# Kernel optimization log

Measured on AMD Instinct MI355X. Metric: run time of the kernel, lower is better.

## Reference

```python
import jax, jax.numpy as jnp
import numpy as np

ALPHA = 2.0   # ATan surrogate alpha (spikingjelly default)
VTH = 0.5     # v_threshold
NUM_HEADS = 8

@jax.custom_vjp
def atan_spike(x):
    return (x >= 0.0).astype(x.dtype)

def _atan_fwd(x):
    return atan_spike(x), x

def _atan_bwd(x, g):
    return (g * (ALPHA / 2.0) / (1.0 + (jnp.pi / 2.0 * ALPHA * x) ** 2),)

atan_spike.defvjp(_atan_fwd, _atan_bwd)

def lif(x, w):
    # ParametricLIFNode, step_mode='m', decay_input=True, v_reset=0 (hard reset), detach_reset
    sg = jax.nn.sigmoid(w)
    def step(v, xt):
        v = v + (xt - v) * sg
        s = atan_spike(v - VTH)
        v = v * (1.0 - jax.lax.stop_gradient(s))  # hard reset to 0, detached
        return v, s
    _, spikes = jax.lax.scan(step, jnp.zeros_like(x[0]), x)
    return spikes

def bn_eT(x, gamma, beta, eps=1e-5):
    # x: [T, B, C, N]; per-(T,C) channel stats over (B, N)  == BatchNorm1d on [B, T*C, N] (train mode)
    T, B, C, N = x.shape
    mean = x.mean(axis=(1, 3), keepdims=True)
    var = jnp.mean((x - mean) ** 2, axis=(1, 3), keepdims=True)
    g = gamma.reshape(T, 1, C, 1)
    b = beta.reshape(T, 1, C, 1)
    return (x - mean) * jax.lax.rsqrt(var + eps) * g + b

def setup_inputs() -> dict:
    key = jax.random.key(0)
    ks = jax.random.split(key, 6)
    T, B, N, C = 16, 8, 196, 512
    return {
        "x": jax.random.normal(ks[0], (T, B, N, C), dtype=jnp.float32),
        "qkv_w": jax.random.normal(ks[1], (3 * C, C), dtype=jnp.float32) * 0.02,
        "qkv_b": jax.random.normal(ks[2], (3 * C,), dtype=jnp.float32) * 0.02,
        "bn1_g": jnp.ones((T * 3 * C,), dtype=jnp.float32),
        "bn1_b": jnp.zeros((T * 3 * C,), dtype=jnp.float32),
        "proj_w": jax.random.normal(ks[3], (C, C), dtype=jnp.float32) * 0.02,
        "proj_b": jax.random.normal(ks[4], (C,), dtype=jnp.float32) * 0.02,
        "bn2_g": jnp.ones((T * C,), dtype=jnp.float32),
        "bn2_b": jnp.zeros((T * C,), dtype=jnp.float32),
        "w_in": jnp.zeros((), dtype=jnp.float32),
        "w_q": jnp.zeros((), dtype=jnp.float32),
        "w_k": jnp.zeros((), dtype=jnp.float32),
        "w_v": jnp.zeros((), dtype=jnp.float32),
        "w_proj": jnp.zeros((), dtype=jnp.float32),
    }

def reference(x, qkv_w, qkv_b, bn1_g, bn1_b, proj_w, proj_b, bn2_g, bn2_b,
              w_in, w_q, w_k, w_v, w_proj):
    T, B, N, C = x.shape
    H = NUM_HEADS
    hd = C // H
    scale = hd ** -0.5

    x = lif(x, w_in)                                            # [T,B,N,C] spikes
    qkv = jnp.einsum('tbnc,oc->tbno', x, qkv_w) + qkv_b         # [T,B,N,3C]
    qkv = bn_eT(jnp.swapaxes(qkv, -2, -1), bn1_g, bn1_b)        # [T,B,3C,N]
    qkv = jnp.swapaxes(qkv, -2, -1).reshape(T, B, N, 3, H, hd)
    qkv = jnp.transpose(qkv, (3, 0, 1, 4, 2, 5))                # [3,T,B,H,N,hd]

    q_sk = lif(qkv[0], w_q)
    k_sk = lif(qkv[1], w_k)
    v_sk = lif(qkv[2], w_v)

    kv = jnp.einsum('tbhnd,tbhne->tbhde', k_sk, v_sk)           # k^T @ v : [T,B,H,hd,hd]
    out = jnp.einsum('tbhnd,tbhde->tbhne', q_sk, kv) * scale    # [T,B,H,N,hd]
    out = jnp.transpose(out, (0, 1, 3, 2, 4)).reshape(T, B, N, C)

    out = lif(out, w_proj)
    out = jnp.einsum('tbnc,oc->tbno', out, proj_w) + proj_b     # [T,B,N,C]
    out = bn_eT(jnp.swapaxes(out, -2, -1), bn2_g, bn2_b)        # [T,B,C,N]
    return jnp.swapaxes(out, -2, -1)                            # [T,B,N,C]
```

## Files before the change

### kernel.cpp

```cpp
#include <hip/hip_runtime.h>


#define TT 16
#define BB 8
#define NNQ 196
#define CC 512
#define HH 8
#define HD 64
#define O3 1536
#define BN (BB*NNQ)
#define PT (BN*CC)
#define WTOT ((O3+CC)*CC)
#define NRG 14

static constexpr float VTH = 0.5f;
typedef __attribute__((ext_vector_type(8))) short short8;
typedef __attribute__((ext_vector_type(4))) float f32x4;
typedef unsigned short u16;

__device__ __forceinline__ float sigm(float w){ return 1.f/(1.f+expf(-w)); }

__device__ __forceinline__ float lif_step(float x, float& v, float sg){
  float d  = __fsub_rn(x, v);
  float dd = __fmul_rn(d, sg);
  v = __fadd_rn(v, dd);
  float sp = (v >= VTH) ? 1.f : 0.f;
  v = __fmul_rn(v, __fsub_rn(1.f, sp));
  return sp;
}

__device__ __forceinline__ u16 bf16_rn(float x){
  unsigned u = __float_as_uint(x);
  unsigned r = u + 0x7FFF + ((u>>16)&1);
  return (u16)(r>>16);
}
__device__ __forceinline__ float bf16_to_f(u16 h){
  return __uint_as_float(((unsigned)h)<<16);
}

__device__ __forceinline__ void gld_lds16(const void* g, void* l){
  __builtin_amdgcn_global_load_lds(
    (const __attribute__((address_space(1))) unsigned int*)g,
    (__attribute__((address_space(3))) unsigned int*)l, 16, 0, 0);
}

__global__ void k_wsplit(const float* __restrict__ qkv_w, const float* __restrict__ proj_w,
                         u16* __restrict__ whi, u16* __restrict__ wmid, u16* __restrict__ wlo){
  int i = blockIdx.x*256 + threadIdx.x;
  float w = (i < O3*CC) ? qkv_w[i] : proj_w[i - O3*CC];
  u16 h = bf16_rn(w);          float r1 = w - bf16_to_f(h);
  u16 m = bf16_rn(r1);         float r2 = r1 - bf16_to_f(m);
  u16 l = bf16_rn(r2);
  whi[i]=h; wmid[i]=m; wlo[i]=l;
}

__global__ void k_lif_x(const float* __restrict__ x, const float* __restrict__ w,
                        float* __restrict__ vin, u16* __restrict__ s0, int t0, int tc){
  int g = blockIdx.x*256 + threadIdx.x;
  float sg = sigm(w[0]);
  float v = (t0==0) ? 0.f : vin[g];
  for (int tt=0; tt<tc; ++tt){
    float sp = lif_step(x[(size_t)(t0+tt)*PT + g], v, sg);
    s0[(size_t)tt*PT + g] = (sp!=0.f) ? 0x3F80 : 0;
  }
  vin[g] = v;
}

template<int ON>
__global__ __launch_bounds__(256)
void k_gemm_mfma(const u16* __restrict__ A, const u16* __restrict__ Wh,
                 const u16* __restrict__ Wm, const u16* __restrict__ Wl,
                 const float* __restrict__ bias, float* __restrict__ Cm, int M){
  __shared__ __align__(16) u16 Al[128][64];
  __shared__ __align__(16) u16 Bh[128][64];
  __shared__ __align__(16) u16 Bm[128][64];
  __shared__ __align__(16) u16 Bl[128][64];
  const int nON = ON/128;
  int nwg = gridDim.x;
  int bid = blockIdx.x;
  int q = nwg >> 3, r = nwg & 7;
  int xcd = bid & 7, idx = bid >> 3;
  int wgid = (xcd < r ? xcd*(q+1) : r*(q+1) + (xcd-r)*q) + idx;
  int mb = wgid / nON, ob = wgid - mb*nON;
  int m0 = mb*128, o0 = ob*128;

  int tid = threadIdx.x;
  int w = tid>>6, lane = tid&63;
  int wm = (w&1)*64, wn = (w>>1)*64;
  int r16 = lane&15, kg = lane>>4;
  int lrow = w*32 + (lane>>3);
  int lslot = lane&7;
  f32x4 acc[4][4] = {};
  for (int k0=0;k0<512;k0+=64){
    #pragma unroll
    for (int i=0;i<4;++i){
      int row = lrow + i*8;
      int gslot = lslot ^ (row&7);
      int gr = m0+row; if (gr>=M) gr=M-1;
      gld_lds16(&A [(size_t)gr*512       + k0 + gslot*8], &Al[w*32+i*8][0]);
      gld_lds16(&Wh[(size_t)(o0+row)*512 + k0 + gslot*8], &Bh[w*32+i*8][0]);
      gld_lds16(&Wm[(size_t)(o0+row)*512 + k0 + gslot*8], &Bm[w*32+i*8][0]);
      gld_lds16(&Wl[(size_t)(o0+row)*512 + k0 + gslot*8], &Bl[w*32+i*8][0]);
    }
    __syncthreads();
    #pragma unroll
    for (int s=0;s<2;++s){
      short8 af[4], bh[4], bm[4], bl[4];
      #pragma unroll
      for (int mt=0;mt<4;++mt){
        int rr = wm + mt*16 + r16;
        af[mt] = *(const short8*)&Al[rr][((s*4+kg)^(rr&7))*8];
      }
      #pragma unroll
      for (int nt=0;nt<4;++nt){
        int rr = wn + nt*16 + r16;
        int sl = ((s*4+kg)^(rr&7))*8;
        bh[nt] = *(const short8*)&Bh[rr][sl];
        bm[nt] = *(const short8*)&Bm[rr][sl];
        bl[nt] = *(const short8*)&Bl[rr][sl];
      }
      #pragma unroll
      for (int mt=0;mt<4;++mt)
        #pragma unroll
        for (int nt=0;nt<4;++nt){
          acc[mt][nt] = __builtin_amdgcn_mfma_f32_16x16x32_bf16(af[mt], bh[nt], acc[mt][nt],0,0,0);
          acc[mt][nt] = __builtin_amdgcn_mfma_f32_16x16x32_bf16(af[mt], bm[nt], acc[mt][nt],0,0,0);
          acc[mt][nt] = __builtin_amdgcn_mfma_f32_16x16x32_bf16(af[mt], bl[nt], acc[mt][nt],0,0,0);
        }
    }
    __syncthreads();
  }
  #pragma unroll
  for (int mt=0; mt<4; ++mt)
    #pragma unroll
    for (int nt=0; nt<4; ++nt){
      int o = o0 + wn + nt*16 + r16;
      float bs = bias[o];
      #pragma unroll
      for (int i=0;i<4;++i){
        int m = m0 + wm + mt*16 + kg*4 + i;
        if (m < M) Cm[(size_t)m*ON + o] = acc[mt][nt][i] + bs;
      }
    }
}

template<int O>
__global__ void k_stat_part(const float* __restrict__ X, double* __restrict__ psum,
                            double* __restrict__ psq){
  int o = blockIdx.x*64 + threadIdx.x;
  int tt = blockIdx.y;
  int rg = blockIdx.z;
  const float* Xb = X + (size_t)tt*BN*O;
  int r0 = rg*112;
  double sum=0.0, sq=0.0;
  for (int i=r0+threadIdx.y; i<r0+112; i+=4){
    double v = (double)Xb[(size_t)i*O + o];
    sum += v; sq += v*v;
  }
  __shared__ double ssum[4][64], ssq[4][64];
  ssum[threadIdx.y][threadIdx.x]=sum;
  ssq [threadIdx.y][threadIdx.x]=sq;
  __syncthreads();
  if (threadIdx.y==0){
    double s = ssum[0][threadIdx.x]+ssum[1][threadIdx.x]+ssum[2][threadIdx.x]+ssum[3][threadIdx.x];
    double q = ssq [0][threadIdx.x]+ssq [1][threadIdx.x]+ssq [2][threadIdx.x]+ssq [3][threadIdx.x];
    size_t idx = ((size_t)tt*O + o)*NRG + rg;
    psum[idx]=s; psq[idx]=q;
  }
}

template<int O, int TCN>
__global__ void k_stat_reduce(const double* __restrict__ psum, const double* __restrict__ psq,
                              float* __restrict__ mean, float* __restrict__ rstd){
  int i = blockIdx.x*256 + threadIdx.x;
  if (i >= TCN*O) return;
  double s=0.0, q=0.0;
  #pragma unroll
  for (int g=0; g<NRG; ++g){ s += psum[(size_t)i*NRG+g]; q += psq[(size_t)i*NRG+g]; }
  double m = s*(1.0/BN);
  double var = q*(1.0/BN) - m*m;
  mean[i]=(float)m;
  rstd[i]=(float)(1.0/sqrt(var+1e-5));
}

__global__ void k_lif_qkv(const float* __restrict__ qkv, const float* __restrict__ mean,
                          const float* __restrict__ rstd, const float* __restrict__ g1,
                          const float* __restrict__ b1,
                          const float* __restrict__ wq, const float* __restrict__ wk,
                          const float* __restrict__ wv,
                          float* __restrict__ vq, float* __restrict__ vk, float* __restrict__ vv,
                          u16* __restrict__ qs, u16* __restrict__ ks,
                          u16* __restrict__ vs, int t0, int tc){
  int g = blockIdx.x*256 + threadIdx.x;
  int j = blockIdx.y;
  int d = g & 63;
  int n = (g>>6) % NNQ;
  int h = (g/(NNQ*64)) & 7;
  int b = g/(NNQ*64*8);
  int o = j*CC + h*HD + d;
  const float* w = (j==0)? wq : (j==1)? wk : wv;
  float* st  = (j==0)? vq : (j==1)? vk : vv;
  u16* out = (j==0)? qs : (j==1)? ks : vs;
  float sg = sigm(w[0]);
  float v = (t0==0) ? 0.f : st[g];
  size_t row = (size_t)(b*NNQ + n)*O3 + o;
  for (int tt=0; tt<tc; ++tt){
    float xv = qkv[(size_t)tt*BN*O3 + row];
    int so = tt*O3 + o;
    int go = (t0+tt)*O3 + o;
    float xn = __fadd_rn(__fmul_rn(__fmul_rn(__fsub_rn(xv, mean[so]), rstd[so]),
                                   g1[go]), b1[go]);
    float sp = lif_step(xn, v, sg);
    out[(size_t)tt*PT + g] = (sp!=0.f) ? 0x3F80 : 0;
  }
  st[g] = v;
}

__global__ __launch_bounds__(256)
void k_kvqv_mfma(const u16* __restrict__ ks, const u16* __restrict__ vs,
                 const u16* __restrict__ qs, float* __restrict__ attn){
  __shared__ __align__(16) u16 Kb[224][64];
  __shared__ __align__(16) u16 Vb[224][64];
  __shared__ __align__(16) u16 kvb[64][64];
  int blk = blockIdx.x;
  size_t base = (size_t)blk * (NNQ*HD);
  int tid = threadIdx.x, w = tid>>6, lane = tid&63;
  int r16 = lane&15, kg = lane>>4;
  for (int u=tid; u<224*8; u+=256){
    int row=u>>3, slot=u&7;
    float4 z = {0.f,0.f,0.f,0.f};
    float4 kd = z, vd = z;
    if (row < NNQ){
      kd = *(const float4*)&ks[base + (size_t)row*64 + slot*8];
      vd = *(const float4*)&vs[base + (size_t)row*64 + slot*8];
    }
    *(float4*)&Kb[row][slot*8] = kd;
    *(float4*)&Vb[row][slot*8] = vd;
  }
  __syncthreads();
  f32x4 acc[4] = {};
  int d0 = w*16;
  for (int n0=0;n0<224;n0+=32){
    short8 af;
    #pragma unroll
    for (int jj=0;jj<8;++jj) af[jj] = (short)Kb[n0+kg*8+jj][d0 + r16];
    #pragma unroll
    for (int nt=0;nt<4;++nt){
      short8 bf;
      #pragma unroll
      for (int jj=0;jj<8;++jj) bf[jj] = (short)Vb[n0+kg*8+jj][nt*16 + r16];
      acc[nt] = __builtin_amdgcn_mfma_f32_16x16x32_bf16(af, bf, acc[nt],0,0,0);
    }
  }
  #pragma unroll
  for (int nt=0;nt<4;++nt)
    #pragma unroll
    for (int i=0;i<4;++i)
      kvb[d0 + kg*4 + i][nt*16 + r16] = (u16)(__float_as_uint(acc[nt][i])>>16);
  __syncthreads();
  for (int u=tid; u<224*8; u+=256){
    int row=u>>3, slot=u&7;
    int sl = slot ^ (row&7);
    float4 qd = {0.f,0.f,0.f,0.f};
    if (row < NNQ) qd = *(const float4*)&qs[base + (size_t)row*64 + slot*8];
    *(float4*)&Kb[row][sl*8] = qd;
  }
  __syncthreads();
  short8 bkv[2][4];
  #pragma unroll
  for (int s=0;s<2;++s)
    #pragma unroll
    for (int nt=0;nt<4;++nt){
      short8 bf;
      #pragma unroll
      for (int jj=0;jj<8;++jj) bf[jj] = (short)kvb[s*32 + kg*8 + jj][nt*16 + r16];
      bkv[s][nt] = bf;
    }
  for (int mt=w; mt<13; mt+=4){
    f32x4 a2[4] = {};
    short8 qa[2];
    #pragma unroll
    for (int s=0;s<2;++s){
      int rr = mt*16 + r16;
      qa[s] = *(const short8*)&Kb[rr][(((s*4+kg)^(rr&7)))*8];
    }
    #pragma unroll
    for (int s=0;s<2;++s)
      #pragma unroll
      for (int nt=0;nt<4;++nt)
        a2[nt] = __builtin_amdgcn_mfma_f32_16x16x32_bf16(qa[s], bkv[s][nt], a2[nt],0,0,0);
    #pragma unroll
    for (int nt=0;nt<4;++nt){
      int e = nt*16 + r16;
      #pragma unroll
      for (int i=0;i<4;++i){
        int n = mt*16 + kg*4 + i;
        if (n < NNQ) attn[base + (size_t)n*64 + e] = a2[nt][i]*0.125f;
      }
    }
  }
}

__global__ void k_lif_attn(const float* __restrict__ ain, const float* __restrict__ w,
                           float* __restrict__ vo, u16* __restrict__ sp, int t0, int tc){
  int g = blockIdx.x*256 + threadIdx.x;
  int e = g & 63;
  int n = (g>>6) % NNQ;
  int h = (g/(NNQ*64)) & 7;
  int b = g/(NNQ*64*8);
  size_t dst = (size_t)(b*NNQ + n)*CC + h*HD + e;
  float sg = sigm(w[0]);
  float v = (t0==0) ? 0.f : vo[g];
  for (int tt=0; tt<tc; ++tt){
    float s = lif_step(ain[(size_t)tt*PT + g], v, sg);
    sp[(size_t)tt*PT + dst] = (s!=0.f) ? 0x3F80 : 0;
  }
  vo[g] = v;
}

__global__ void k_bn2_apply(const float* __restrict__ X, const float* __restrict__ mean,
                            const float* __restrict__ rstd, const float* __restrict__ g2,
                            const float* __restrict__ b2, float* __restrict__ Y, int t0){
  size_t idx = ((size_t)blockIdx.x*256 + threadIdx.x)*4;
  int tt = (int)(idx / PT);
  size_t off = idx - (size_t)tt*PT;
  int c = (int)(off & (CC-1));
  float4 xv = *(const float4*)&X[idx];
  float4 mv = *(const float4*)&mean[tt*CC + c];
  float4 rv = *(const float4*)&rstd[tt*CC + c];
  float4 gv = *(const float4*)&g2[(t0+tt)*CC + c];
  float4 bv = *(const float4*)&b2[(t0+tt)*CC + c];
  float4 yv;
  yv.x = __fadd_rn(__fmul_rn(__fmul_rn(__fsub_rn(xv.x, mv.x), rv.x), gv.x), bv.x);
  yv.y = __fadd_rn(__fmul_rn(__fmul_rn(__fsub_rn(xv.y, mv.y), rv.y), gv.y), bv.y);
  yv.z = __fadd_rn(__fmul_rn(__fmul_rn(__fsub_rn(xv.z, mv.z), rv.z), gv.z), bv.z);
  yv.w = __fadd_rn(__fmul_rn(__fmul_rn(__fsub_rn(xv.w, mv.w), rv.w), gv.w), bv.w);
  *(float4*)&Y[(size_t)(t0+tt)*PT + off] = yv;
}

extern "C" void kernel_launch(void* const* d_in, const int* in_sizes, int n_in,
                              void* d_out, int out_size, void* d_ws, size_t ws_size,
                              hipStream_t stream){
  const float* x      = (const float*)d_in[0];
  const float* qkv_w  = (const float*)d_in[1];
  const float* qkv_b  = (const float*)d_in[2];
  const float* bn1_g  = (const float*)d_in[3];
  const float* bn1_b  = (const float*)d_in[4];
  const float* proj_w = (const float*)d_in[5];
  const float* proj_b = (const float*)d_in[6];
  const float* bn2_g  = (const float*)d_in[7];
  const float* bn2_b  = (const float*)d_in[8];
  const float* w_in   = (const float*)d_in[9];
  const float* w_q    = (const float*)d_in[10];
  const float* w_k    = (const float*)d_in[11];
  const float* w_v    = (const float*)d_in[12];
  const float* w_proj = (const float*)d_in[13];
  float* outp = (float*)d_out;

  auto need = [](int tc)->size_t{
    return 4ull*5*PT + 8ull*tc*O3 + 8ull*tc*CC
         + 16ull*tc*O3*NRG + 16ull*tc*CC*NRG
         + 6ull*WTOT
         + 10ull*tc*PT
         + 4ull*tc*BN*O3;
  };
  int TC = 16;
  while (TC > 1 && need(TC) > ws_size) TC >>= 1;

  char* p = (char*)d_ws;
  float* vin = (float*)p; p += 4ull*PT;
  float* vq  = (float*)p; p += 4ull*PT;
  float* vk  = (float*)p; p += 4ull*PT;
  float* vv  = (float*)p; p += 4ull*PT;
  float* vo  = (float*)p; p += 4ull*PT;
  float* mean1 = (float*)p; p += 4ull*TC*O3;
  float* rstd1 = (float*)p; p += 4ull*TC*O3;
  float* mean2 = (float*)p; p += 4ull*TC*CC;
  float* rstd2 = (float*)p; p += 4ull*TC*CC;
  double* p1sum = (double*)p; p += 8ull*TC*O3*NRG;
  double* p1sq  = (double*)p; p += 8ull*TC*O3*NRG;
  double* p2sum = (double*)p; p += 8ull*TC*CC*NRG;
  double* p2sq  = (double*)p; p += 8ull*TC*CC*NRG;
  u16* whi  = (u16*)p; p += 2ull*WTOT;
  u16* wmid = (u16*)p; p += 2ull*WTOT;
  u16* wlo  = (u16*)p; p += 2ull*WTOT;
  u16* s0    = (u16*)p; p += 2ull*TC*PT;
  u16* qsb   = (u16*)p; p += 2ull*TC*PT;
  u16* ksb   = (u16*)p; p += 2ull*TC*PT;
  u16* vsb   = (u16*)p; p += 2ull*TC*PT;
  u16* sproj = (u16*)p; p += 2ull*TC*PT;
  float* qkv_all = (float*)p;
  float* attn    = qkv_all;
  float* projo   = qkv_all + (size_t)TC*PT;

  k_wsplit<<<WTOT/256, 256, 0, stream>>>(qkv_w, proj_w, whi, wmid, wlo);

  for (int t0=0; t0<TT; t0+=TC){
    int M = TC*BN;
    int nMB = (M+127)/128;
    k_lif_x<<<PT/256, 256, 0, stream>>>(x, w_in, vin, s0, t0, TC);

    k_gemm_mfma<O3><<<nMB*(O3/128), 256, 0, stream>>>(
        s0, whi, wmid, wlo, qkv_b, qkv_all, M);

    k_stat_part<O3><<<dim3(O3/64, TC, NRG), dim3(64,4), 0, stream>>>(qkv_all, p1sum, p1sq);
    if (TC == 16)
      k_stat_reduce<O3,16><<<(16*O3+255)/256, 256, 0, stream>>>(p1sum, p1sq, mean1, rstd1);
    else if (TC == 8)
      k_stat_reduce<O3,8><<<(8*O3+255)/256, 256, 0, stream>>>(p1sum, p1sq, mean1, rstd1);
    else
      k_stat_reduce<O3,4><<<(4*O3+255)/256, 256, 0, stream>>>(p1sum, p1sq, mean1, rstd1);

    k_lif_qkv<<<dim3(PT/256, 3), 256, 0, stream>>>(qkv_all, mean1, rstd1, bn1_g, bn1_b,
                                                   w_q, w_k, w_v, vq, vk, vv,
                                                   qsb, ksb, vsb, t0, TC);

    k_kvqv_mfma<<<TC*BB*HH, 256, 0, stream>>>(ksb, vsb, qsb, attn);

    k_lif_attn<<<PT/256, 256, 0, stream>>>(attn, w_proj, vo, sproj, t0, TC);

    k_gemm_mfma<CC><<<nMB*(CC/128), 256, 0, stream>>>(
        sproj, whi + (size_t)O3*CC, wmid + (size_t)O3*CC, wlo + (size_t)O3*CC,
        proj_b, projo, M);

    k_stat_part<CC><<<dim3(CC/64, TC, NRG), dim3(64,4), 0, stream>>>(projo, p2sum, p2sq);
    if (TC == 16)
      k_stat_reduce<CC,16><<<(16*CC+255)/256, 256, 0, stream>>>(p2sum, p2sq, mean2, rstd2);
    else if (TC == 8)
      k_stat_reduce<CC,8><<<(8*CC+255)/256, 256, 0, stream>>>(p2sum, p2sq, mean2, rstd2);
    else
      k_stat_reduce<CC,4><<<(4*CC+255)/256, 256, 0, stream>>>(p2sum, p2sq, mean2, rstd2);

    k_bn2_apply<<<(TC*(size_t)PT)/1024, 256, 0, stream>>>(projo, mean2, rstd2,
                                                          bn2_g, bn2_b, outp, t0);
  }
}
```

Before: 410.9 us.

## Fuse BatchNorm partial statistics into GEMM epilogue and enlarge QKV M-tile

The GEMM epilogue now accumulates per-column sum and sum-of-squares in double, split by time-step segment, and writes per-M-block partials. A new fold kernel then combines them into mean and rstd, replacing the separate stat_part kernel that re-read the whole GEMM output. The QKV GEMM also uses a 256-row M tile, and launch bounds now request 2 blocks per SM. This removes a full extra pass over the large qkv and proj outputs. In exchange it adds register pressure and an LDS reduction to the GEMM epilogue, and assumes an M tile spans at most two time segments.

Result: slower. 435.4 us (+6.0%).

```diff
diff --git a/kernel.cpp b/kernel.cpp
--- a/kernel.cpp
+++ b/kernel.cpp
@@ -11,7 +11,6 @@
 #define BN (BB*NNQ)
 #define PT (BN*CC)
 #define WTOT ((O3+CC)*CC)
-#define NRG 14
 
 static constexpr float VTH = 0.5f;
 typedef __attribute__((ext_vector_type(8))) short short8;
@@ -66,12 +65,14 @@
   vin[g] = v;
 }
 
-template<int ON>
-__global__ __launch_bounds__(256)
+template<int ON, int MT>
+__global__ __launch_bounds__(256, 2)
 void k_gemm_mfma(const u16* __restrict__ A, const u16* __restrict__ Wh,
                  const u16* __restrict__ Wm, const u16* __restrict__ Wl,
-                 const float* __restrict__ bias, float* __restrict__ Cm, int M){
-  __shared__ __align__(16) u16 Al[128][64];
+                 const float* __restrict__ bias, float* __restrict__ Cm,
+                 double* __restrict__ psum, double* __restrict__ psq, int M){
+  constexpr int MTn = MT/32;
+  __shared__ __align__(16) u16 Al[MT][64];
   __shared__ __align__(16) u16 Bh[128][64];
   __shared__ __align__(16) u16 Bm[128][64];
   __shared__ __align__(16) u16 Bl[128][64];
@@ -82,22 +83,28 @@
   int xcd = bid & 7, idx = bid >> 3;
   int wgid = (xcd < r ? xcd*(q+1) : r*(q+1) + (xcd-r)*q) + idx;
   int mb = wgid / nON, ob = wgid - mb*nON;
-  int m0 = mb*128, o0 = ob*128;
+  int m0 = mb*MT, o0 = ob*128;
 
   int tid = threadIdx.x;
   int w = tid>>6, lane = tid&63;
-  int wm = (w&1)*64, wn = (w>>1)*64;
+  int wm = (w&1)*(MT/2), wn = (w>>1)*64;
   int r16 = lane&15, kg = lane>>4;
-  int lrow = w*32 + (lane>>3);
+  int lrowB = w*32 + (lane>>3);
+  int lrowA = w*(MT/4) + (lane>>3);
   int lslot = lane&7;
-  f32x4 acc[4][4] = {};
+  f32x4 acc[MTn][4] = {};
   for (int k0=0;k0<512;k0+=64){
     #pragma unroll
-    for (int i=0;i<4;++i){
-      int row = lrow + i*8;
+    for (int i=0;i<MT/32;++i){
+      int row = lrowA + i*8;
       int gslot = lslot ^ (row&7);
       int gr = m0+row; if (gr>=M) gr=M-1;
-      gld_lds16(&A [(size_t)gr*512       + k0 + gslot*8], &Al[w*32+i*8][0]);
+      gld_lds16(&A[(size_t)gr*512 + k0 + gslot*8], &Al[w*(MT/4)+i*8][0]);
+    }
+    #pragma unroll
+    for (int i=0;i<4;++i){
+      int row = lrowB + i*8;
+      int gslot = lslot ^ (row&7);
       gld_lds16(&Wh[(size_t)(o0+row)*512 + k0 + gslot*8], &Bh[w*32+i*8][0]);
       gld_lds16(&Wm[(size_t)(o0+row)*512 + k0 + gslot*8], &Bm[w*32+i*8][0]);
       gld_lds16(&Wl[(size_t)(o0+row)*512 + k0 + gslot*8], &Bl[w*32+i*8][0]);
@@ -105,12 +112,7 @@
     __syncthreads();
     #pragma unroll
     for (int s=0;s<2;++s){
-      short8 af[4], bh[4], bm[4], bl[4];
-      #pragma unroll
-      for (int mt=0;mt<4;++mt){
-        int rr = wm + mt*16 + r16;
-        af[mt] = *(const short8*)&Al[rr][((s*4+kg)^(rr&7))*8];
-      }
+      short8 bh[4], bm[4], bl[4];
       #pragma unroll
       for (int nt=0;nt<4;++nt){
         int rr = wn + nt*16 + r16;
@@ -120,67 +122,92 @@
         bl[nt] = *(const short8*)&Bl[rr][sl];
       }
       #pragma unroll
-      for (int mt=0;mt<4;++mt)
+      for (int mt=0;mt<MTn;++mt){
+        int rr = wm + mt*16 + r16;
+        short8 af = *(const short8*)&Al[rr][((s*4+kg)^(rr&7))*8];
         #pragma unroll
         for (int nt=0;nt<4;++nt){
-          acc[mt][nt] = __builtin_amdgcn_mfma_f32_16x16x32_bf16(af[mt], bh[nt], acc[mt][nt],0,0,0);
-          acc[mt][nt] = __builtin_amdgcn_mfma_f32_16x16x32_bf16(af[mt], bm[nt], acc[mt][nt],0,0,0);
-          acc[mt][nt] = __builtin_amdgcn_mfma_f32_16x16x32_bf16(af[mt], bl[nt], acc[mt][nt],0,0,0);
+          acc[mt][nt] = __builtin_amdgcn_mfma_f32_16x16x32_bf16(af, bh[nt], acc[mt][nt],0,0,0);
+          acc[mt][nt] = __builtin_amdgcn_mfma_f32_16x16x32_bf16(af, bm[nt], acc[mt][nt],0,0,0);
+          acc[mt][nt] = __builtin_amdgcn_mfma_f32_16x16x32_bf16(af, bl[nt], acc[mt][nt],0,0,0);
         }
+      }
     }
     __syncthreads();
   }
+  int bseg = (m0/1568 + 1)*1568;
+  double ssm[4][2] = {}, ssq2[4][2] = {};
   #pragma unroll
-  for (int mt=0; mt<4; ++mt)
-    #pragma unroll
-    for (int nt=0; nt<4; ++nt){
-      int o = o0 + wn + nt*16 + r16;
-      float bs = bias[o];
+  for (int nt=0; nt<4; ++nt){
+    int o = o0 + wn + nt*16 + r16;
+    float bs = bias[o];
+    #pragma unroll
+    for (int mt=0; mt<MTn; ++mt){
       #pragma unroll
       for (int i=0;i<4;++i){
         int m = m0 + wm + mt*16 + kg*4 + i;
-        if (m < M) Cm[(size_t)m*ON + o] = acc[mt][nt][i] + bs;
+        if (m < M){
+          float val = acc[mt][nt][i] + bs;
+          Cm[(size_t)m*ON + o] = val;
+          int sg = (m >= bseg) ? 1 : 0;
+          ssm[nt][sg]  += (double)val;
+          ssq2[nt][sg] += (double)val*(double)val;
+        }
       }
     }
-}
-
-template<int O>
-__global__ void k_stat_part(const float* __restrict__ X, double* __restrict__ psum,
-                            double* __restrict__ psq){
-  int o = blockIdx.x*64 + threadIdx.x;
-  int tt = blockIdx.y;
-  int rg = blockIdx.z;
-  const float* Xb = X + (size_t)tt*BN*O;
-  int r0 = rg*112;
-  double sum=0.0, sq=0.0;
-  for (int i=r0+threadIdx.y; i<r0+112; i+=4){
-    double v = (double)Xb[(size_t)i*O + o];
-    sum += v; sq += v*v;
-  }
-  __shared__ double ssum[4][64], ssq[4][64];
-  ssum[threadIdx.y][threadIdx.x]=sum;
-  ssq [threadIdx.y][threadIdx.x]=sq;
+  }
+  #pragma unroll
+  for (int nt=0;nt<4;++nt)
+    #pragma unroll
+    for (int sg=0;sg<2;++sg){
+      ssm[nt][sg]  += __shfl_xor(ssm[nt][sg], 16);
+      ssm[nt][sg]  += __shfl_xor(ssm[nt][sg], 32);
+      ssq2[nt][sg] += __shfl_xor(ssq2[nt][sg], 16);
+      ssq2[nt][sg] += __shfl_xor(ssq2[nt][sg], 32);
+    }
+  double* statd = (double*)&Al[0][0];
+  if (lane < 16){
+    #pragma unroll
+    for (int nt=0;nt<4;++nt)
+      #pragma unroll
+      for (int sg=0;sg<2;++sg){
+        int bi = (((w*4+nt)*16 + r16)*2 + sg)*2;
+        statd[bi+0] = ssm[nt][sg];
+        statd[bi+1] = ssq2[nt][sg];
+      }
+  }
   __syncthreads();
-  if (threadIdx.y==0){
-    double s = ssum[0][threadIdx.x]+ssum[1][threadIdx.x]+ssum[2][threadIdx.x]+ssum[3][threadIdx.x];
-    double q = ssq [0][threadIdx.x]+ssq [1][threadIdx.x]+ssq [2][threadIdx.x]+ssq [3][threadIdx.x];
-    size_t idx = ((size_t)tt*O + o)*NRG + rg;
-    psum[idx]=s; psq[idx]=q;
-  }
-}
-
-template<int O, int TCN>
-__global__ void k_stat_reduce(const double* __restrict__ psum, const double* __restrict__ psq,
-                              float* __restrict__ mean, float* __restrict__ rstd){
+  {
+    int sg = tid & 1, ol = tid >> 1;
+    int nh = ol>>6, ntv = (ol&63)>>4, rv = ol&15;
+    int i0 = ((((2*nh+0)*4+ntv)*16 + rv)*2 + sg)*2;
+    int i1 = ((((2*nh+1)*4+ntv)*16 + rv)*2 + sg)*2;
+    size_t pi = ((size_t)mb*2 + sg)*ON + o0 + ol;
+    psum[pi] = statd[i0+0] + statd[i1+0];
+    psq [pi] = statd[i0+1] + statd[i1+1];
+  }
+}
+
+template<int O, int MT>
+__global__ void k_stat_fold(const double* __restrict__ psum, const double* __restrict__ psq,
+                            float* __restrict__ mean, float* __restrict__ rstd,
+                            int nmb, int total){
   int i = blockIdx.x*256 + threadIdx.x;
-  if (i >= TCN*O) return;
-  double s=0.0, q=0.0;
-  #pragma unroll
-  for (int g=0; g<NRG; ++g){ s += psum[(size_t)i*NRG+g]; q += psq[(size_t)i*NRG+g]; }
+  if (i >= total) return;
+  int tt = i / O, o = i - tt*O;
+  double s=0.0, qq=0.0;
+  for (int mb=0; mb<nmb; ++mb){
+    int tb = (mb*MT)/1568;
+    int sg = tt - tb;
+    if (sg==0 || sg==1){
+      size_t pi = ((size_t)mb*2 + sg)*O + o;
+      s += psum[pi]; qq += psq[pi];
+    }
+  }
   double m = s*(1.0/BN);
-  double var = q*(1.0/BN) - m*m;
-  mean[i]=(float)m;
-  rstd[i]=(float)(1.0/sqrt(var+1e-5));
+  double var = qq*(1.0/BN) - m*m;
+  mean[i] = (float)m;
+  rstd[i] = (float)(1.0/sqrt(var+1e-5));
 }
 
 __global__ void k_lif_qkv(const float* __restrict__ qkv, const float* __restrict__ mean,
@@ -358,14 +385,18 @@
   float* outp = (float*)d_out;
 
   auto need = [](int tc)->size_t{
-    return 4ull*5*PT + 8ull*tc*O3 + 8ull*tc*CC
-         + 16ull*tc*O3*NRG + 16ull*tc*CC*NRG
+    int nmb1 = (tc*BN + 255)/256;
+    int nmb2 = (tc*BN + 127)/128;
+    return 4ull*5*PT + 4ull*tc*O3*2 + 4ull*tc*CC*2
+         + 16ull*nmb1*2*O3 + 16ull*nmb2*2*CC
          + 6ull*WTOT
          + 10ull*tc*PT
          + 4ull*tc*BN*O3;
   };
   int TC = 16;
   while (TC > 1 && need(TC) > ws_size) TC >>= 1;
+  int nmb1 = (TC*BN + 255)/256;
+  int nmb2 = (TC*BN + 127)/128;
 
   char* p = (char*)d_ws;
   float* vin = (float*)p; p += 4ull*PT;
@@ -377,10 +408,10 @@
   float* rstd1 = (float*)p; p += 4ull*TC*O3;
   float* mean2 = (float*)p; p += 4ull*TC*CC;
   float* rstd2 = (float*)p; p += 4ull*TC*CC;
-  double* p1sum = (double*)p; p += 8ull*TC*O3*NRG;
-  double* p1sq  = (double*)p; p += 8ull*TC*O3*NRG;
-  double* p2sum = (double*)p; p += 8ull*TC*CC*NRG;
-  double* p2sq  = (double*)p; p += 8ull*TC*CC*NRG;
+  double* p1sum = (double*)p; p += 8ull*nmb1*2*O3;
+  double* p1sq  = (double*)p; p += 8ull*nmb1*2*O3;
+  double* p2sum = (double*)p; p += 8ull*nmb2*2*CC;
+  double* p2sq  = (double*)p; p += 8ull*nmb2*2*CC;
   u16* whi  = (u16*)p; p += 2ull*WTOT;
   u16* wmid = (u16*)p; p += 2ull*WTOT;
   u16* wlo  = (u16*)p; p += 2ull*WTOT;
@@ -397,19 +428,13 @@
 
   for (int t0=0; t0<TT; t0+=TC){
     int M = TC*BN;
-    int nMB = (M+127)/128;
     k_lif_x<<<PT/256, 256, 0, stream>>>(x, w_in, vin, s0, t0, TC);
 
-    k_gemm_mfma<O3><<<nMB*(O3/128), 256, 0, stream>>>(
-        s0, whi, wmid, wlo, qkv_b, qkv_all, M);
-
-    k_stat_part<O3><<<dim3(O3/64, TC, NRG), dim3(64,4), 0, stream>>>(qkv_all, p1sum, p1sq);
-    if (TC == 16)
-      k_stat_reduce<O3,16><<<(16*O3+255)/256, 256, 0, stream>>>(p1sum, p1sq, mean1, rstd1);
-    else if (TC == 8)
-      k_stat_reduce<O3,8><<<(8*O3+255)/256, 256, 0, stream>>>(p1sum, p1sq, mean1, rstd1);
-    else
-      k_stat_reduce<O3,4><<<(4*O3+255)/256, 256, 0, stream>>>(p1sum, p1sq, mean1, rstd1);
+    k_gemm_mfma<O3,256><<<nmb1*(O3/128), 256, 0, stream>>>(
+        s0, whi, wmid, wlo, qkv_b, qkv_all, p1sum, p1sq, M);
+
+    k_stat_fold<O3,256><<<(TC*O3+255)/256, 256, 0, stream>>>(
+        p1sum, p1sq, mean1, rstd1, nmb1, TC*O3);
 
     k_lif_qkv<<<dim3(PT/256, 3), 256, 0, stream>>>(qkv_all, mean1, rstd1, bn1_g, bn1_b,
                                                    w_q, w_k, w_v, vq, vk, vv,
@@ -419,17 +444,12 @@
 
     k_lif_attn<<<PT/256, 256, 0, stream>>>(attn, w_proj, vo, sproj, t0, TC);
 
-    k_gemm_mfma<CC><<<nMB*(CC/128), 256, 0, stream>>>(
+    k_gemm_mfma<CC,128><<<nmb2*(CC/128), 256, 0, stream>>>(
         sproj, whi + (size_t)O3*CC, wmid + (size_t)O3*CC, wlo + (size_t)O3*CC,
-        proj_b, projo, M);
-
-    k_stat_part<CC><<<dim3(CC/64, TC, NRG), dim3(64,4), 0, stream>>>(projo, p2sum, p2sq);
-    if (TC == 16)
-      k_stat_reduce<CC,16><<<(16*CC+255)/256, 256, 0, stream>>>(p2sum, p2sq, mean2, rstd2);
-    else if (TC == 8)
-      k_stat_reduce<CC,8><<<(8*CC+255)/256, 256, 0, stream>>>(p2sum, p2sq, mean2, rstd2);
-    else
-      k_stat_reduce<CC,4><<<(4*CC+255)/256, 256, 0, stream>>>(p2sum, p2sq, mean2, rstd2);
+        proj_b, projo, p2sum, p2sq, M);
+
+    k_stat_fold<CC,128><<<(TC*CC+255)/256, 256, 0, stream>>>(
+        p2sum, p2sq, mean2, rstd2, nmb2, TC*CC);
 
     k_bn2_apply<<<(TC*(size_t)PT)/1024, 256, 0, stream>>>(projo, mean2, rstd2,
                                                           bn2_g, bn2_b, outp, t0);
```
